# Performance work log

Hardware: AMD Instinct MI355X
Metric: run time of the kernel (lower is better)

Reference implementation:

```python
import jax, jax.numpy as jnp
import numpy as np

B, D, R = 256, 4096, 16
MAX_R = 2 * R - 1  # static upper bound on radius; per-row steps masked by r_mask


def setup_inputs() -> dict:
    key = jax.random.key(0)
    kx, kw, kb = jax.random.split(key, 3)
    x = (jax.random.uniform(kx, (B, D)) < 0.5).astype(jnp.float32)  # random bits
    A = jax.random.normal(kw, (D, D), dtype=jnp.float32) * 0.01
    W = (A + A.T) * 0.5  # symmetric quadratic coupling
    bias = jax.random.normal(kb, (D,), dtype=jnp.float32) * 0.1
    return {"x": x, "W": W, "bias": bias}


def reference(x, W, bias):
    # energy model: score(x) = 0.5 * x' W x + b' x  (per batch row)
    score_fn = lambda z: 0.5 * jnp.einsum('bd,de,be->b', z, W, z) + z @ bias
    grad_fn = jax.grad(lambda z: score_fn(z).sum())

    key = jax.random.key(42)
    k_rad, k_samp, k_acc = jax.random.split(key, 3)
    radius = jax.random.randint(k_rad, (B, 1), 1, 2 * R)
    r_mask = (jnp.arange(MAX_R)[None, :] < radius).astype(x.dtype)  # [B, MAX_R]

    score_x = score_fn(x)                                  # [B]
    grad_x = jax.lax.stop_gradient(grad_fn(x))             # detach as in torch
    score_change_x = (1.0 - 2.0 * x) * grad_x * 0.5        # [B, D] proposal logits

    b_idx = jnp.arange(B)

    def body(carry, inp):
        cur_x, blocked = carry
        k, m = inp  # per-step RNG key, per-step mask column [B]
        idx = jax.random.categorical(k, score_change_x + blocked)  # multinomial w/ zeroed probs
        cur_bits = cur_x[b_idx, idx]
        cur_x = cur_x.at[b_idx, idx].set(m * (1.0 - cur_bits) + (1.0 - m) * cur_bits)
        blocked = blocked.at[b_idx, idx].set(-jnp.inf)  # prob_x[b, idx] = 0
        return (cur_x, blocked), idx

    keys = jax.random.split(k_samp, MAX_R)
    (y, _), idx_steps = jax.lax.scan(body, (x, jnp.zeros_like(x)), (keys, r_mask.T))
    idx_all = idx_steps.T  # [B, MAX_R]

    score_y = score_fn(y)
    grad_y = jax.lax.stop_gradient(grad_fn(y))
    score_change_y = (1.0 - 2.0 * y) * grad_y * 0.5

    # masked log-softmax tensors: step j's proposal excludes indices flipped at other steps
    oh = jax.nn.one_hot(idx_all, D, dtype=x.dtype)        # [B, MAX_R, D]
    cum = jnp.cumsum(oh, axis=1)
    before = cum - oh                                      # indices sampled at steps i < j
    after = cum[:, -1:, :] - cum                           # indices sampled at steps i > j
    change_fwd = jnp.where(before > 0, -jnp.inf, score_change_x[:, None, :])
    change_bwd = jnp.where(after > 0, -jnp.inf, score_change_y[:, None, :])

    g_fwd = jnp.take_along_axis(jax.nn.log_softmax(change_fwd, axis=-1), idx_all[:, :, None], axis=2)[..., 0]
    g_bwd = jnp.take_along_axis(jax.nn.log_softmax(change_bwd, axis=-1), idx_all[:, :, None], axis=2)[..., 0]
    log_fwd = jnp.sum(g_fwd * r_mask, axis=-1) + score_x
    log_bwd = jnp.sum(g_bwd * r_mask, axis=-1) + score_y

    log_acc = log_bwd - log_fwd
    u = jax.random.uniform(k_acc, (B,))
    accepted = (jnp.exp(log_acc) >= u).astype(x.dtype)[:, None]  # [B, 1]
    y_sg = jax.lax.stop_gradient(y)
    acc_sg = jax.lax.stop_gradient(accepted)
    return y_sg * acc_sg + (1.0 - acc_sg) * x
```

## Files before the change

### kernel.cpp

```cpp
#include <hip/hip_runtime.h>
#include <math.h>

#define BB 256
#define DD 4096
#define MAXR 31
#define NCAND 4
#define CAPG 192
#define U_THRESH 0.9778f
#define GUARD 4.0f

typedef unsigned short u16;
typedef u16 u16x8 __attribute__((ext_vector_type(8)));
typedef __bf16 bf16x8 __attribute__((ext_vector_type(8)));
typedef float f32x16 __attribute__((ext_vector_type(16)));

__device__ __forceinline__ void tf2x32(unsigned k0, unsigned k1, unsigned c0, unsigned c1,
                                       unsigned &o0, unsigned &o1) {
  unsigned ks2 = k0 ^ k1 ^ 0x1BD11BDAu;
  unsigned x0 = c0 + k0;
  unsigned x1 = c1 + k1;
#define TF_ROT(v, r) (((v) << (r)) | ((v) >> (32 - (r))))
#define TF_R(r) { x0 += x1; x1 = TF_ROT(x1, r); x1 ^= x0; }
  TF_R(13) TF_R(15) TF_R(26) TF_R(6)   x0 += k1;  x1 += ks2 + 1u;
  TF_R(17) TF_R(29) TF_R(16) TF_R(24)  x0 += ks2; x1 += k0 + 2u;
  TF_R(13) TF_R(15) TF_R(26) TF_R(6)   x0 += k0;  x1 += k1 + 3u;
  TF_R(17) TF_R(29) TF_R(16) TF_R(24)  x0 += k1;  x1 += ks2 + 4u;
  TF_R(13) TF_R(15) TF_R(26) TF_R(6)   x0 += ks2; x1 += k0 + 5u;
#undef TF_R
#undef TF_ROT
  o0 = x0; o1 = x1;
}

__device__ __forceinline__ unsigned tf_xor(unsigned k0, unsigned k1, unsigned c0, unsigned c1) {
  unsigned a, b; tf2x32(k0, k1, c0, c1, a, b); return a ^ b;
}

__device__ __forceinline__ float bits_to_unit(unsigned bits) {
  return __uint_as_float(0x3f800000u | (bits >> 9)) - 1.0f;
}

__device__ __forceinline__ void keys_of(int j, unsigned &kk0, unsigned &kk1) {
  unsigned ks0, ks1;
  tf2x32(0u, 42u, 0u, 1u, ks0, ks1);
  tf2x32(ks0, ks1, 0u, (unsigned)j, kk0, kk1);
}

__device__ __forceinline__ int radius_of(int b) {
  unsigned krad0, krad1, k10, k11, k20, k21;
  tf2x32(0u, 42u, 0u, 0u, krad0, krad1);
  tf2x32(krad0, krad1, 0u, 0u, k10, k11);
  tf2x32(krad0, krad1, 0u, 1u, k20, k21);
  unsigned hi = tf_xor(k10, k11, 0u, (unsigned)b);
  unsigned lo = tf_xor(k20, k21, 0u, (unsigned)b);
  return 1 + (int)(((hi % 31u) * 4u + (lo % 31u)) % 31u);
}

__device__ __forceinline__ float uacc_of(int b) {
  unsigned ka0, ka1;
  tf2x32(0u, 42u, 0u, 2u, ka0, ka1);
  return bits_to_unit(tf_xor(ka0, ka1, 0u, (unsigned)b));
}

__device__ __forceinline__ double dlog(double x) {
  unsigned long long ub = (unsigned long long)__double_as_longlong(x);
  int e = (int)((ub >> 52) & 0x7FFull) - 1022;
  double m = __longlong_as_double((long long)((ub & 0x000FFFFFFFFFFFFFull) | 0x3FE0000000000000ull));
  if (m < 0.70710678118654752440) { m *= 2.0; e -= 1; }
  double r = (m - 1.0) / (m + 1.0);
  double z = r * r;
  double s = fma(z, fma(z, fma(z, fma(z, fma(z, fma(z, 1.0/15.0, 1.0/13.0),
                1.0/11.0), 1.0/9.0), 1.0/7.0), 1.0/5.0), 1.0/3.0);
  double t2 = 2.0 * r;
  return fma((double)e, 0.69314718055994530942, fma(t2 * z, s, t2));
}

__device__ __forceinline__ float gumbel_from_u(float f) {
  float uu = (f == 0.0f) ? 1.17549435e-38f : f;
  float t1 = (float)dlog((double)uu);
  return -(float)dlog((double)(-t1));
}

__device__ __forceinline__ float gumbel_of(unsigned kk0, unsigned kk1, unsigned n) {
  return gumbel_from_u(bits_to_unit(tf_xor(kk0, kk1, 0u, n)));
}

__device__ __forceinline__ double blockReduce1024(double v, double* lds) {
  int t = threadIdx.x;
  #pragma unroll
  for (int off = 32; off > 0; off >>= 1) v += __shfl_down(v, off);
  __syncthreads();
  if ((t & 63) == 0) lds[t >> 6] = v;
  __syncthreads();
  double s = 0.0;
  #pragma unroll
  for (int i = 0; i < 16; i++) s += lds[i];
  return s;
}

__device__ __forceinline__ void split3(float w, u16 &h, u16 &l, u16 &q) {
  __bf16 hb = (__bf16)w;
  float r = w - (float)hb;
  __bf16 lb = (__bf16)r;
  float r2 = r - (float)lb;
  __bf16 qb = (__bf16)r2;
  h = __builtin_bit_cast(u16, hb);
  l = __builtin_bit_cast(u16, lb);
  q = __builtin_bit_cast(u16, qb);
}

__global__ __launch_bounds__(256, 2) void k_gemm(
    const float* __restrict__ x, const float* __restrict__ W,
    float* __restrict__ Cpart, int klen) {
  int t = threadIdx.x;
  int g = blockIdx.x;
  int nt = g & 63, mt = (g >> 6) & 1, kc = g >> 7;
  int k0 = kc * klen;

  __shared__ alignas(16) u16 As[4][128][8];
  __shared__ alignas(16) u16 Bs[3][4][64][8];

  const float* xrow = x + (size_t)(mt * 128) * DD + k0;
  const float* wrow = W + (size_t)(nt * 64) * DD + k0;

  int am = t >> 2, akg = t & 3;
  int bn = t >> 2, bkg = t & 3;

  float4 aR0, aR1, aR2, aR3;
  float4 bR0, bR1;
  int nsteps = klen / 32;

  {
    const float* ap = xrow + (size_t)am * DD + akg * 8;
    aR0 = *(const float4*)ap;       aR1 = *(const float4*)(ap + 4);
    const float* ap2 = ap + (size_t)64 * DD;
    aR2 = *(const float4*)ap2;      aR3 = *(const float4*)(ap2 + 4);
    const float* wp = wrow + (size_t)bn * DD + bkg * 8;
    bR0 = *(const float4*)wp;       bR1 = *(const float4*)(wp + 4);
  }

  int wid = t >> 6, lane = t & 63;
  int wr = (wid >> 1) * 64, wc = (wid & 1) * 32;
  int lm = lane & 31, lh = lane >> 5;

  f32x16 acc[2];
  #pragma unroll
  for (int i = 0; i < 2; i++)
    #pragma unroll
    for (int r = 0; r < 16; r++) acc[i][r] = 0.0f;

  for (int s = 0; s < nsteps; s++) {
    __syncthreads();
    {
      float af32[8];
      *(float4*)&af32[0] = aR0; *(float4*)&af32[4] = aR1;
      u16x8 av;
      #pragma unroll
      for (int i = 0; i < 8; i++) av[i] = __builtin_bit_cast(u16, (__bf16)af32[i]);
      *(u16x8*)&As[akg][am][0] = av;
      *(float4*)&af32[0] = aR2; *(float4*)&af32[4] = aR3;
      #pragma unroll
      for (int i = 0; i < 8; i++) av[i] = __builtin_bit_cast(u16, (__bf16)af32[i]);
      *(u16x8*)&As[akg][am + 64][0] = av;
    }
    {
      float wv[8];
      *(float4*)&wv[0] = bR0; *(float4*)&wv[4] = bR1;
      u16x8 ph, pl, pq;
      #pragma unroll
      for (int i = 0; i < 8; i++) {
        u16 hh, ll, qq;
        split3(wv[i], hh, ll, qq);
        ph[i] = hh; pl[i] = ll; pq[i] = qq;
      }
      *(u16x8*)&Bs[0][bkg][bn][0] = ph;
      *(u16x8*)&Bs[1][bkg][bn][0] = pl;
      *(u16x8*)&Bs[2][bkg][bn][0] = pq;
    }
    __syncthreads();
    if (s + 1 < nsteps) {
      int kk = (s + 1) * 32;
      const float* ap = xrow + (size_t)am * DD + kk + akg * 8;
      aR0 = *(const float4*)ap;       aR1 = *(const float4*)(ap + 4);
      const float* ap2 = ap + (size_t)64 * DD;
      aR2 = *(const float4*)ap2;      aR3 = *(const float4*)(ap2 + 4);
      const float* wp = wrow + (size_t)bn * DD + kk + bkg * 8;
      bR0 = *(const float4*)wp;       bR1 = *(const float4*)(wp + 4);
    }
    bf16x8 af[2][2];
    #pragma unroll
    for (int mf = 0; mf < 2; mf++)
      #pragma unroll
      for (int h = 0; h < 2; h++)
        af[mf][h] = *(const bf16x8*)&As[2 * h + lh][wr + mf * 32 + lm][0];
    #pragma unroll
    for (int p = 0; p < 3; p++) {
      bf16x8 b0 = *(const bf16x8*)&Bs[p][lh][wc + lm][0];
      bf16x8 b1 = *(const bf16x8*)&Bs[p][2 + lh][wc + lm][0];
      #pragma unroll
      for (int mf = 0; mf < 2; mf++) {
        acc[mf] = __builtin_amdgcn_mfma_f32_32x32x16_bf16(af[mf][0], b0, acc[mf], 0, 0, 0);
        acc[mf] = __builtin_amdgcn_mfma_f32_32x32x16_bf16(af[mf][1], b1, acc[mf], 0, 0, 0);
      }
    }
  }

  float* Cp = Cpart + (size_t)kc * ((size_t)BB * DD);
  #pragma unroll
  for (int mf = 0; mf < 2; mf++) {
    int col   = nt * 64 + wc + lm;
    int rbase = mt * 128 + wr + mf * 32 + 4 * lh;
    #pragma unroll
    for (int r = 0; r < 16; r++) {
      int row = rbase + (r & 3) + 8 * (r >> 2);
      Cp[(size_t)row * DD + col] = acc[mf][r];
    }
  }
}

__global__ __launch_bounds__(256) void k_filter(
    u16* __restrict__ flt_list, int* __restrict__ flt_cnt) {
  int t = threadIdx.x;
  int fb = blockIdx.x;
  int b = fb / MAXR, j = fb % MAXR;
  unsigned kk0, kk1;
  keys_of(j, kk0, kk1);
  unsigned base_c = (unsigned)(b * DD);
  const unsigned KMIN = (unsigned)ceil((double)U_THRESH * 8388608.0);

  __shared__ int fcnt;
  __shared__ u16 fl[CAPG];
  if (t == 0) fcnt = 0;
  __syncthreads();

  #pragma unroll
  for (int p = 0; p < 16; p++) {
    int d = t + 256 * p;
    unsigned bits = tf_xor(kk0, kk1, 0u, base_c + (unsigned)d);
    if ((bits >> 9) >= KMIN) {
      int pos = atomicAdd(&fcnt, 1);
      if (pos < CAPG) fl[pos] = (u16)d;
    }
  }
  __syncthreads();
  int n = fcnt;
  if (t == 0) flt_cnt[fb] = n;
  int nstore = n < CAPG ? n : CAPG;
  if (t < nstore) flt_list[(size_t)fb * CAPG + t] = fl[t];
}

__global__ __launch_bounds__(1024) void k_tail(
    const float* __restrict__ Cpart, const float* __restrict__ bias,
    const float* __restrict__ x, const float* __restrict__ W,
    const u16* __restrict__ flt_list, const int* __restrict__ flt_cnt,
    float* __restrict__ out, int KS) {
  int b = blockIdx.x, t = threadIdx.x;

  __shared__ float sc_lds[DD];
  __shared__ float gr_lds[DD];
  __shared__ double redbuf[16];
  __shared__ float lmx[16];
  __shared__ float ls_v[16];
  __shared__ int   ls_i[16];
  __shared__ int   win_i[4];
  __shared__ int   cand_lds[MAXR][NCAND];
  __shared__ int   fb_list[MAXR];
  __shared__ int   nfb_s;
  __shared__ int   fidx[MAXR];
  __shared__ float fsgn[MAXR];
  __shared__ unsigned mask[DD / 32];
  __shared__ int   pick_s;
  __shared__ int   nf_s;
  __shared__ float scmax_s;
  __shared__ double score_x_s, score_y_s, Ssum_s, Tsum_s;
  __shared__ float scx_s[MAXR], scy_s[MAXR];
  __shared__ float accf;

  int d0 = t * 4;
  size_t o = (size_t)b * DD + d0;
  float a0 = 0.f, a1 = 0.f, a2 = 0.f, a3 = 0.f;
  for (int kc = 0; kc < KS; kc++) {
    float4 c = *(const float4*)&Cpart[(size_t)kc * BB * DD + o];
    a0 += c.x; a1 += c.y; a2 += c.z; a3 += c.w;
  }
  float4 bv4 = *(const float4*)&bias[d0];
  float4 xv4 = *(const float4*)&x[o];
  float gg[4] = { a0 + bv4.x, a1 + bv4.y, a2 + bv4.z, a3 + bv4.w };
  float xx[4] = { xv4.x, xv4.y, xv4.z, xv4.w };
  float bb[4] = { bv4.x, bv4.y, bv4.z, bv4.w };
  float scv[4];
  double s1 = 0.0, s2 = 0.0;
  float mx = -INFINITY;
  #pragma unroll
  for (int k = 0; k < 4; k++) {
    scv[k] = (1.0f - 2.0f * xx[k]) * gg[k] * 0.5f;
    mx = fmaxf(mx, scv[k]);
    s1 += (double)xx[k] * (double)gg[k];
    s2 += (double)xx[k] * (double)bb[k];
  }
  *(float4*)&sc_lds[d0] = *(float4*)&scv[0];
  *(float4*)&gr_lds[d0] = *(float4*)&gg[0];
  if (t < 128) mask[t] = 0u;
  if (t == 0) { nf_s = radius_of(b); nfb_s = 0; }
  double sx = exp((double)scv[0]) + exp((double)scv[1]) + exp((double)scv[2]) + exp((double)scv[3]);
  double S1 = blockReduce1024(s1, redbuf);
  double S2 = blockReduce1024(s2, redbuf);
  double Sv = blockReduce1024(sx, redbuf);
  #pragma unroll
  for (int off = 32; off > 0; off >>= 1) mx = fmaxf(mx, __shfl_down(mx, off));
  __syncthreads();
  if ((t & 63) == 0) lmx[t >> 6] = mx;
  __syncthreads();
  if (t == 0) {
    float m = lmx[0];
    #pragma unroll
    for (int i = 1; i < 16; i++) m = fmaxf(m, lmx[i]);
    score_x_s = 0.5 * (S1 + S2);
    scmax_s = m;
    Ssum_s = Sv;
  }
  __syncthreads();

  {
    int wv = t >> 6, ln = t & 63;
    float scmax_l = scmax_s;
    for (int pass = 0; pass < 2; pass++) {
      int j = pass * 16 + wv;
      if (j < MAXR) {
        unsigned kk0, kk1;
        keys_of(j, kk0, kk1);
        int n = flt_cnt[b * MAXR + j];
        bool fastok = !(n > CAPG || n < NCAND);
        float v4 = -INFINITY;
        if (fastok) {
          const u16* fl = &flt_list[(size_t)(b * MAXR + j) * CAPG];
          float vv[3]; int dd[3]; unsigned alive = 0u;
          #pragma unroll
          for (int q = 0; q < 3; q++) {
            int idx = ln + 64 * q;
            if (idx < n) {
              int d = (int)fl[idx];
              float f = bits_to_unit(tf_xor(kk0, kk1, 0u, (unsigned)(b * DD) + (unsigned)d));
              vv[q] = sc_lds[d] + gumbel_from_u(f);
              dd[q] = d;
              alive |= 1u << q;
            } else { vv[q] = -INFINITY; dd[q] = 0x7FFFFFFF; }
          }
          for (int r = 0; r < NCAND; r++) {
            float bv = -INFINITY; int bi = 0x7FFFFFFF;
            #pragma unroll
            for (int q = 0; q < 3; q++)
              if (((alive >> q) & 1u) && (vv[q] > bv || (vv[q] == bv && dd[q] < bi))) { bv = vv[q]; bi = dd[q]; }
            #pragma unroll
            for (int off = 1; off < 64; off <<= 1) {
              float ov = __shfl_xor(bv, off);
              int   oi = __shfl_xor(bi, off);
              if (ov > bv || (ov == bv && oi < bi)) { bv = ov; bi = oi; }
            }
            if (ln == 0) cand_lds[j][r] = bi;
            v4 = bv;
            #pragma unroll
            for (int q = 0; q < 3; q++) if (dd[q] == bi) alive &= ~(1u << q);
          }
        }
        if (ln == 0) {
          bool needfb = !fastok || (v4 < scmax_l + GUARD);
          if (needfb) fb_list[atomicAdd(&nfb_s, 1)] = j;
        }
      }
    }
  }
  __syncthreads();

  int nfb = nfb_s;
  for (int fi = 0; fi < nfb; fi++) {
    int j = fb_list[fi];
    unsigned kk0, kk1;
    keys_of(j, kk0, kk1);
    float vq[4]; int dq[4];
    unsigned alive = 0xFu;
    #pragma unroll
    for (int q = 0; q < 4; q++) {
      int d = t * 4 + q;
      vq[q] = sc_lds[d] + gumbel_of(kk0, kk1, (unsigned)(b * DD + d));
      dq[q] = d;
    }
    for (int r = 0; r < NCAND; r++) {
      float lv = -INFINITY; int li = 0x7FFFFFFF;
      #pragma unroll
      for (int q = 0; q < 4; q++)
        if (((alive >> q) & 1u) && (vq[q] > lv || (vq[q] == lv && dq[q] < li))) { lv = vq[q]; li = dq[q]; }
      #pragma unroll
      for (int off = 32; off > 0; off >>= 1) {
        float ov = __shfl_down(lv, off);
        int   oi = __shfl_down(li, off);
        if (ov > lv || (ov == lv && oi < li)) { lv = ov; li = oi; }
      }
      if ((t & 63) == 0) { ls_v[t >> 6] = lv; ls_i[t >> 6] = li; }
      __syncthreads();
      if (t == 0) {
        float fv = ls_v[0]; int fi2 = ls_i[0];
        #pragma unroll
        for (int w = 1; w < 16; w++)
          if (ls_v[w] > fv || (ls_v[w] == fv && ls_i[w] < fi2)) { fv = ls_v[w]; fi2 = ls_i[w]; }
        cand_lds[j][r] = fi2;
        win_i[0] = fi2;
      }
      __syncthreads();
      int wi = win_i[0];
      #pragma unroll
      for (int q = 0; q < 4; q++) if (dq[q] == wi) alive &= ~(1u << q);
    }
    __syncthreads();
  }

  int jdone = 0;
  while (true) {
    if (t == 0) {
      int j = jdone;
      while (j < MAXR) {
        int pick = -1;
        #pragma unroll
        for (int r = 0; r < NCAND; r++) {
          int idx = cand_lds[j][r];
          if (pick < 0 && !((mask[idx >> 5] >> (idx & 31)) & 1u)) pick = idx;
        }
        if (pick < 0) break;
        fidx[j] = pick;
        mask[pick >> 5] |= (1u << (pick & 31));
        j++;
      }
      pick_s = j;
    }
    __syncthreads();
    int jf = pick_s;
    if (jf >= MAXR) break;
    {
      unsigned kk0, kk1;
      keys_of(jf, kk0, kk1);
      float lv = -INFINITY; int li = 0x7FFFFFFF;
      #pragma unroll
      for (int q = 0; q < 4; q++) {
        int d = t * 4 + q;
        if ((mask[d >> 5] >> (d & 31)) & 1u) continue;
        float vv = sc_lds[d] + gumbel_of(kk0, kk1, (unsigned)(b * DD + d));
        if (vv > lv || (vv == lv && d < li)) { lv = vv; li = d; }
      }
      #pragma unroll
      for (int off = 32; off > 0; off >>= 1) {
        float ov = __shfl_down(lv, off);
        int   oi = __shfl_down(li, off);
        if (ov > lv || (ov == lv && oi < li)) { lv = ov; li = oi; }
      }
      if ((t & 63) == 0) { ls_v[t >> 6] = lv; ls_i[t >> 6] = li; }
      __syncthreads();
      if (t == 0) {
        float fv = ls_v[0]; int fi2 = ls_i[0];
        #pragma unroll
        for (int w = 1; w < 16; w++)
          if (ls_v[w] > fv || (ls_v[w] == fv && ls_i[w] < fi2)) { fv = ls_v[w]; fi2 = ls_i[w]; }
        fidx[jf] = fi2;
        mask[fi2 >> 5] |= (1u << (fi2 & 31));
      }
      __syncthreads();
    }
    jdone = jf + 1;
  }

  int nf = nf_s;
  if (t < nf) fsgn[t] = 1.0f - 2.0f * x[(size_t)b * DD + fidx[t]];
  __syncthreads();

  float gd[4] = { gr_lds[d0], gr_lds[d0 + 1], gr_lds[d0 + 2], gr_lds[d0 + 3] };
  float yy[4] = { xx[0], xx[1], xx[2], xx[3] };
  for (int jj = 0; jj < nf; jj++) {
    int fd = fidx[jj];
    float s = fsgn[jj];
    float4 wv = *(const float4*)&W[(size_t)fd * DD + d0];
    gd[0] = fmaf(s, wv.x, gd[0]);
    gd[1] = fmaf(s, wv.y, gd[1]);
    gd[2] = fmaf(s, wv.z, gd[2]);
    gd[3] = fmaf(s, wv.w, gd[3]);
    int r = fd - d0;
    if (r >= 0 && r < 4) yy[r] = 1.0f - xx[r];
  }
  float scy[4];
  double t1 = 0.0, t2 = 0.0;
  #pragma unroll
  for (int k = 0; k < 4; k++) {
    scy[k] = (1.0f - 2.0f * yy[k]) * gd[k] * 0.5f;
    t1 += (double)yy[k] * (double)gd[k];
    t2 += (double)yy[k] * (double)bb[k];
  }
  double sy = exp((double)scy[0]) + exp((double)scy[1]) + exp((double)scy[2]) + exp((double)scy[3]);
  __syncthreads();
  *(float4*)&gr_lds[d0] = *(float4*)&scy[0];
  double T1 = blockReduce1024(t1, redbuf);
  double T2 = blockReduce1024(t2, redbuf);
  double Tv = blockReduce1024(sy, redbuf);
  if (t == 0) { score_y_s = 0.5 * (T1 + T2); Tsum_s = Tv; }
  __syncthreads();

  if (t < MAXR) {
    int id = fidx[t];
    scx_s[t] = sc_lds[id];
    scy_s[t] = gr_lds[id];
  }
  __syncthreads();
  if (t < 32) {
    int lane = t;
    double S = Ssum_s, T = Tsum_s;
    double ex = (t < MAXR) ? exp((double)scx_s[t]) : 0.0;
    double scn = ex;
    #pragma unroll
    for (int off = 1; off < 32; off <<= 1) {
      double ov = __shfl_up(scn, off);
      if (lane >= off) scn += ov;
    }
    double pre = scn - ex;
    double gf = (t < nf) ? ((double)scx_s[t] - dlog(S - pre)) : 0.0;
    double ey = (t < MAXR) ? exp((double)scy_s[t]) : 0.0;
    double scn2 = ey;
    #pragma unroll
    for (int off = 1; off < 32; off <<= 1) {
      double ov = __shfl_down(scn2, off);
      if (lane + off < 32) scn2 += ov;
    }
    double suf = scn2 - ey;
    double gb = (t < nf) ? ((double)scy_s[t] - dlog(T - suf)) : 0.0;
    #pragma unroll
    for (int off = 16; off > 0; off >>= 1) {
      gf += __shfl_down(gf, off);
      gb += __shfl_down(gb, off);
    }
    if (t == 0) {
      double log_acc = (gb + score_y_s) - (gf + score_x_s);
      accf = (exp(log_acc) >= (double)uacc_of(b)) ? 1.0f : 0.0f;
    }
  }
  __syncthreads();
  float a = accf;
  float4 ov4;
  ov4.x = a * yy[0] + (1.0f - a) * xx[0];
  ov4.y = a * yy[1] + (1.0f - a) * xx[1];
  ov4.z = a * yy[2] + (1.0f - a) * xx[2];
  ov4.w = a * yy[3] + (1.0f - a) * xx[3];
  *(float4*)&out[o] = ov4;
}

extern "C" void kernel_launch(void* const* d_in, const int* in_sizes, int n_in,
                              void* d_out, int out_size, void* d_ws, size_t ws_size,
                              hipStream_t stream) {
  const float* x    = (const float*)d_in[0];
  const float* W    = (const float*)d_in[1];
  const float* bias = (const float*)d_in[2];
  float* out = (float*)d_out;
  char* ws = (char*)d_ws;
  const size_t MB = 1ull << 20;

  u16*    flt_list = (u16*)(ws + 0*MB);
  int*    flt_cnt  = (int*)(ws + 3*MB);
  float*  Cpart    = (float*)(ws + 4*MB);

  size_t base = 4*MB;
  int KS = 1;
  if      (ws_size >= base + 16*MB) KS = 4;
  else if (ws_size >= base +  8*MB) KS = 2;

  int NG = 64 * 2 * KS;

  k_filter<<<BB*MAXR, 256, 0, stream>>>(flt_list, flt_cnt);
  k_gemm  <<<NG, 256, 0, stream>>>(x, W, Cpart, DD/KS);
  k_tail  <<<BB, 1024, 0, stream>>>(Cpart, bias, x, W, flt_list, flt_cnt, out, KS);
}
```

Baseline: 238.2 us.

## Fuse Gumbel threshold filter into tail kernel with per-wave LDS staging

Removes the separate k_filter launch and its global list and count buffers. Each wave of k_tail now generates the Threefry bits for its step over the full row, filters them against the threshold and stages the surviving indices and raw bits in LDS, so the bits are not regenerated when the candidates are scored. The rotate macro is replaced with a builtin rotate. This saves one launch and the global round trip, but the RNG work now runs on only 256 blocks instead of 7936, so the tail's serial section gets longer, and the tail uses more LDS.

```diff
diff --git a/kernel.cpp b/kernel.cpp
--- a/kernel.cpp
+++ b/kernel.cpp
@@ -5,7 +5,7 @@
 #define DD 4096
 #define MAXR 31
 #define NCAND 4
-#define CAPG 192
+#define CAPW 192
 #define U_THRESH 0.9778f
 #define GUARD 4.0f
 
@@ -19,15 +19,13 @@
   unsigned ks2 = k0 ^ k1 ^ 0x1BD11BDAu;
   unsigned x0 = c0 + k0;
   unsigned x1 = c1 + k1;
-#define TF_ROT(v, r) (((v) << (r)) | ((v) >> (32 - (r))))
-#define TF_R(r) { x0 += x1; x1 = TF_ROT(x1, r); x1 ^= x0; }
+#define TF_R(r) { x0 += x1; x1 = __builtin_rotateleft32(x1, r); x1 ^= x0; }
   TF_R(13) TF_R(15) TF_R(26) TF_R(6)   x0 += k1;  x1 += ks2 + 1u;
   TF_R(17) TF_R(29) TF_R(16) TF_R(24)  x0 += ks2; x1 += k0 + 2u;
   TF_R(13) TF_R(15) TF_R(26) TF_R(6)   x0 += k0;  x1 += k1 + 3u;
   TF_R(17) TF_R(29) TF_R(16) TF_R(24)  x0 += k1;  x1 += ks2 + 4u;
   TF_R(13) TF_R(15) TF_R(26) TF_R(6)   x0 += ks2; x1 += k0 + 5u;
 #undef TF_R
-#undef TF_ROT
   o0 = x0; o1 = x1;
 }
 
@@ -217,46 +215,17 @@
   }
 }
 
-__global__ __launch_bounds__(256) void k_filter(
-    u16* __restrict__ flt_list, int* __restrict__ flt_cnt) {
-  int t = threadIdx.x;
-  int fb = blockIdx.x;
-  int b = fb / MAXR, j = fb % MAXR;
-  unsigned kk0, kk1;
-  keys_of(j, kk0, kk1);
-  unsigned base_c = (unsigned)(b * DD);
-  const unsigned KMIN = (unsigned)ceil((double)U_THRESH * 8388608.0);
-
-  __shared__ int fcnt;
-  __shared__ u16 fl[CAPG];
-  if (t == 0) fcnt = 0;
-  __syncthreads();
-
-  #pragma unroll
-  for (int p = 0; p < 16; p++) {
-    int d = t + 256 * p;
-    unsigned bits = tf_xor(kk0, kk1, 0u, base_c + (unsigned)d);
-    if ((bits >> 9) >= KMIN) {
-      int pos = atomicAdd(&fcnt, 1);
-      if (pos < CAPG) fl[pos] = (u16)d;
-    }
-  }
-  __syncthreads();
-  int n = fcnt;
-  if (t == 0) flt_cnt[fb] = n;
-  int nstore = n < CAPG ? n : CAPG;
-  if (t < nstore) flt_list[(size_t)fb * CAPG + t] = fl[t];
-}
-
 __global__ __launch_bounds__(1024) void k_tail(
     const float* __restrict__ Cpart, const float* __restrict__ bias,
     const float* __restrict__ x, const float* __restrict__ W,
-    const u16* __restrict__ flt_list, const int* __restrict__ flt_cnt,
     float* __restrict__ out, int KS) {
   int b = blockIdx.x, t = threadIdx.x;
 
   __shared__ float sc_lds[DD];
   __shared__ float gr_lds[DD];
+  __shared__ unsigned stg_b[16][CAPW];
+  __shared__ u16      stg_d[16][CAPW];
+  __shared__ int      wcnt[16];
   __shared__ double redbuf[16];
   __shared__ float lmx[16];
   __shared__ float ls_v[16];
@@ -300,6 +269,7 @@
   *(float4*)&sc_lds[d0] = *(float4*)&scv[0];
   *(float4*)&gr_lds[d0] = *(float4*)&gg[0];
   if (t < 128) mask[t] = 0u;
+  if (t < 16) wcnt[t] = 0;
   if (t == 0) { nf_s = radius_of(b); nfb_s = 0; }
   double sx = exp((double)scv[0]) + exp((double)scv[1]) + exp((double)scv[2]) + exp((double)scv[3]);
   double S1 = blockReduce1024(s1, redbuf);
@@ -323,23 +293,38 @@
   {
     int wv = t >> 6, ln = t & 63;
     float scmax_l = scmax_s;
+    const unsigned KMIN = (unsigned)ceil((double)U_THRESH * 8388608.0);
+    unsigned base_c = (unsigned)(b * DD);
     for (int pass = 0; pass < 2; pass++) {
       int j = pass * 16 + wv;
-      if (j < MAXR) {
-        unsigned kk0, kk1;
+      bool active = (j < MAXR);
+      unsigned kk0 = 0, kk1 = 0;
+      if (active) {
         keys_of(j, kk0, kk1);
-        int n = flt_cnt[b * MAXR + j];
-        bool fastok = !(n > CAPG || n < NCAND);
+        unsigned d = (unsigned)ln;
+        #pragma unroll 8
+        for (int q = 0; q < 64; q++) {
+          unsigned bits = tf_xor(kk0, kk1, 0u, base_c + d);
+          if ((bits >> 9) >= KMIN) {
+            int pos = atomicAdd(&wcnt[wv], 1);
+            if (pos < CAPW) { stg_d[wv][pos] = (u16)d; stg_b[wv][pos] = bits; }
+          }
+          d += 64;
+        }
+      }
+      __syncthreads();
+      if (active) {
+        int n = wcnt[wv];
+        bool fastok = (n <= CAPW) && (n >= NCAND);
         float v4 = -INFINITY;
         if (fastok) {
-          const u16* fl = &flt_list[(size_t)(b * MAXR + j) * CAPG];
           float vv[3]; int dd[3]; unsigned alive = 0u;
           #pragma unroll
           for (int q = 0; q < 3; q++) {
             int idx = ln + 64 * q;
             if (idx < n) {
-              int d = (int)fl[idx];
-              float f = bits_to_unit(tf_xor(kk0, kk1, 0u, (unsigned)(b * DD) + (unsigned)d));
+              int d = (int)stg_d[wv][idx];
+              float f = bits_to_unit(stg_b[wv][idx]);
               vv[q] = sc_lds[d] + gumbel_from_u(f);
               dd[q] = d;
               alive |= 1u << q;
@@ -367,9 +352,11 @@
           if (needfb) fb_list[atomicAdd(&nfb_s, 1)] = j;
         }
       }
-    }
-  }
-  __syncthreads();
+      __syncthreads();
+      if (t < 16) wcnt[t] = 0;
+      __syncthreads();
+    }
+  }
 
   int nfb = nfb_s;
   for (int fi = 0; fi < nfb; fi++) {
@@ -557,18 +544,14 @@
   char* ws = (char*)d_ws;
   const size_t MB = 1ull << 20;
 
-  u16*    flt_list = (u16*)(ws + 0*MB);
-  int*    flt_cnt  = (int*)(ws + 3*MB);
-  float*  Cpart    = (float*)(ws + 4*MB);
-
-  size_t base = 4*MB;
+  float* Cpart = (float*)ws;
+
   int KS = 1;
-  if      (ws_size >= base + 16*MB) KS = 4;
-  else if (ws_size >= base +  8*MB) KS = 2;
+  if      (ws_size >= 16*MB) KS = 4;
+  else if (ws_size >=  8*MB) KS = 2;
 
   int NG = 64 * 2 * KS;
 
-  k_filter<<<BB*MAXR, 256, 0, stream>>>(flt_list, flt_cnt);
-  k_gemm  <<<NG, 256, 0, stream>>>(x, W, Cpart, DD/KS);
-  k_tail  <<<BB, 1024, 0, stream>>>(Cpart, bias, x, W, flt_list, flt_cnt, out, KS);
-}
+  k_gemm<<<NG, 256, 0, stream>>>(x, W, Cpart, DD/KS);
+  k_tail<<<BB, 1024, 0, stream>>>(Cpart, bias, x, W, out, KS);
+}
```

Measured after the change: 255.8 us. +7.4%, slower.
